# Performance work log

Hardware: AMD Instinct MI355X
Metric: run time of the kernel (lower is better)

Reference implementation:

```python
import jax, jax.numpy as jnp
import numpy as np

N, D, R, C_IN = 384, 256, 64, 2
REL_H, NEI_H = 128, 256


def setup_inputs() -> dict:
    key = jax.random.key(0)
    ks = jax.random.split(key, 16)
    inp = {
        "corr_index": jax.random.normal(ks[0], (N, N, C_IN), jnp.float32),
        "nei_index": jax.random.randint(ks[1], (N, N), 0, 2, jnp.int32),
        "nei_num": jax.random.randint(ks[2], (N,), 0, N, jnp.int32),
        "outgate": jax.random.uniform(ks[3], (N, D), jnp.float32),
        "self_h": jax.random.normal(ks[4], (N, D), jnp.float32),
        "self_c": jax.random.normal(ks[5], (N, D), jnp.float32),
        # relativeLayer: 2-layer MLP, relu after both layers (iflastac=True)
        "rel_w1": jax.random.normal(ks[6], (C_IN, REL_H), jnp.float32) * 0.1,
        "rel_b1": jnp.zeros((REL_H,), jnp.float32),
        "rel_w2": jax.random.normal(ks[7], (REL_H, R), jnp.float32) * 0.1,
        "rel_b2": jnp.zeros((R,), jnp.float32),
        # ngate: single Linear(R+2D -> D) + sigmoid
        "ngate_w": jax.random.normal(ks[8], (R + 2 * D, D), jnp.float32) * 0.005,
        "ngate_b": jnp.zeros((D,), jnp.float32),
        # WAr: single Linear(R+2D -> 1), no activation (WAr_ac='')
        "war_w": jax.random.normal(ks[9], (R + 2 * D, 1), jnp.float32) * 0.05,
        "war_b": jnp.zeros((1,), jnp.float32),
        # W_nei: Linear(D->NEI_H)+relu, Linear(NEI_H->D), no last activation
        "wnei_w1": jax.random.normal(ks[10], (D, NEI_H), jnp.float32) * 0.05,
        "wnei_b1": jnp.zeros((NEI_H,), jnp.float32),
        "wnei_w2": jax.random.normal(ks[11], (NEI_H, D), jnp.float32) * 0.05,
        "wnei_b2": jnp.zeros((D,), jnp.float32),
    }
    return inp


def reference(corr_index, nei_index, nei_num, outgate, self_h, self_c,
              rel_w1, rel_b1, rel_w2, rel_b2, ngate_w, ngate_b,
              war_w, war_b, wnei_w1, wnei_b1, wnei_w2, wnei_b2):
    n, d = self_h.shape
    mask = nei_index > 0  # [N, N], pair (i, j)
    # relativeLayer on pairwise relative coords: relu(relu(x W1 + b1) W2 + b2)
    r = jax.nn.relu(jax.nn.relu(corr_index @ rel_w1 + rel_b1) @ rel_w2 + rel_b2)  # [N,N,R]
    # In torch code flat index k = i*N + j: hi_t[k] = self_h[i], nei_inputs[k] = self_h[j]
    h_i = jnp.broadcast_to(self_h[:, None, :], (n, n, d))
    h_j = jnp.broadcast_to(self_h[None, :, :], (n, n, d))
    feat = jnp.concatenate([r, h_i, h_j], axis=-1)  # [N,N,R+2D]
    gate = jax.nn.sigmoid(feat @ ngate_w + ngate_b)  # [N,N,D]
    msg = h_j * gate
    tt = (feat @ war_w + war_b)[..., 0]  # [N,N] attention logits
    # scatter into zero-init matrix, then Pos[Pos==0] = -inf, row softmax
    pos = jnp.where(mask, tt, 0.0)
    pos = jnp.where(pos == 0.0, -jnp.inf, pos)
    pos = jax.nn.softmax(pos, axis=1)  # [N,N]
    # masked, attention-weighted messages; guard NaN from fully-masked rows
    H = jnp.where(mask[:, :, None], msg * pos[:, :, None], 0.0)  # [N,N,D]
    h_sum = jnp.sum(H, axis=1)  # [N,D]
    h_sum = jax.nn.relu(h_sum @ wnei_w1 + wnei_b1) @ wnei_w2 + wnei_b2
    C = h_sum + self_c
    H_out = outgate * jnp.tanh(C)
    return (outgate, H_out, C)
```

## Files before the change

### kernel.cpp

```cpp
#include <hip/hip_runtime.h>
#include <hip/hip_bf16.h>
#include <math.h>

#define N 384
#define D 256
#define R 64
#define RELH 128
#define NN (N*N)
#define ND (N*D)
#define JCHUNK 64
#define NCHUNK (N / JCHUNK)
#define TPB 16
#define LOG2E 1.44269504088896f
#define BHS_STRIDE 132
#define HS_STRIDE 264

typedef _Float16 f16x8 __attribute__((ext_vector_type(8)));
typedef _Float16 f16x2 __attribute__((ext_vector_type(2)));
typedef float f32x4 __attribute__((ext_vector_type(4)));

__device__ __forceinline__ float fast_sigmoid(float x) {
    float e = __builtin_amdgcn_exp2f(-LOG2E * x);
    return __builtin_amdgcn_rcpf(1.f + e);
}
__device__ __forceinline__ float fast_exp(float x) {
    return __builtin_amdgcn_exp2f(LOG2E * x);
}
__device__ __forceinline__ float fast_tanh(float x) {
    float e = __builtin_amdgcn_exp2f(2.f * LOG2E * x);
    return 1.f - 2.f * __builtin_amdgcn_rcpf(1.f + e);
}

__global__ __launch_bounds__(256) void prep_kernel(
        const float* __restrict__ self_h, const float* __restrict__ ngate_w,
        const float* __restrict__ ngate_b, const float* __restrict__ war_w,
        const float* __restrict__ wnei_w1, const float* __restrict__ wnei_w2,
        float* __restrict__ A, float* __restrict__ Bm,
        unsigned int* __restrict__ bh,
        float* __restrict__ u, float* __restrict__ v,
        _Float16* __restrict__ wf,
        _Float16* __restrict__ wf1, _Float16* __restrict__ wf2) {
    int b = blockIdx.x, tid = threadIdx.x;
    int wv = tid >> 6, l = tid & 63;
    int lg = l >> 4, ln = l & 15;

    if (b < 6) {
        int r0 = b * 64 + wv * 16;
        for (int rr = 0; rr < 16; ++rr) {
            int row = r0 + rr;
            float su = 0.f, sv = 0.f;
            #pragma unroll
            for (int k = 0; k < 4; ++k) {
                int d = k * 64 + l;
                float h = self_h[row * D + d];
                su = fmaf(h, war_w[R + d], su);
                sv = fmaf(h, war_w[R + D + d], sv);
            }
            #pragma unroll
            for (int off = 32; off; off >>= 1) {
                su += __shfl_down(su, off);
                sv += __shfl_down(sv, off);
            }
            if (l == 0) { u[row] = su; v[row] = sv; }
        }
    } else if (b < 54) {
        int W = (b - 6) * 4 + wv;
        int m0 = (W >> 3) * 16;
        int cb = (W & 7) * 64;
        const float* wsrc = ngate_w + (size_t)(cb >= 256 ? 320 : 64) * D + (cb & 255);
        f32x4 acc[4];
        #pragma unroll
        for (int nt = 0; nt < 4; ++nt) acc[nt] = (f32x4){0.f, 0.f, 0.f, 0.f};
        #pragma unroll
        for (int s = 0; s < 8; ++s) {
            const float4* hp = (const float4*)&self_h[(size_t)(m0 + ln) * D + s * 32 + lg * 8];
            float4 h0 = hp[0], h1 = hp[1];
            f16x8 af;
            af[0] = (_Float16)h0.x; af[1] = (_Float16)h0.y;
            af[2] = (_Float16)h0.z; af[3] = (_Float16)h0.w;
            af[4] = (_Float16)h1.x; af[5] = (_Float16)h1.y;
            af[6] = (_Float16)h1.z; af[7] = (_Float16)h1.w;
            #pragma unroll
            for (int nt = 0; nt < 4; ++nt) {
                f16x8 bf;
                #pragma unroll
                for (int ii = 0; ii < 8; ++ii)
                    bf[ii] = (_Float16)wsrc[(size_t)(s * 32 + lg * 8 + ii) * D + nt * 16 + ln];
                acc[nt] = __builtin_amdgcn_mfma_f32_16x16x32_f16(af, bf, acc[nt], 0, 0, 0);
            }
        }
        #pragma unroll
        for (int nt = 0; nt < 4; ++nt)
            #pragma unroll
            for (int reg = 0; reg < 4; ++reg) {
                int row = m0 + lg * 4 + reg;
                int col = cb + nt * 16 + ln;
                if (col < 256) {
                    A[row * D + col] = acc[nt][reg] + ngate_b[col];
                } else {
                    int c2 = col - 256;
                    float bmv = acc[nt][reg];
                    Bm[row * D + c2] = bmv;
                    f16x2 pk;
                    pk[0] = (_Float16)bmv;
                    pk[1] = (_Float16)self_h[row * D + c2];
                    bh[row * D + c2] = __builtin_bit_cast(unsigned int, pk);
                }
            }
    } else if (b < 62) {
        int blkEq = (b - 54) * 4 + wv;
        int s = blkEq >> 4, t = blkEq & 15;
        #pragma unroll
        for (int ii = 0; ii < 8; ++ii) {
            float w = ngate_w[(s * 32 + lg * 8 + ii) * D + t * 16 + ln];
            wf[((size_t)(s * 16 + t) * 64 + l) * 8 + ii] = (_Float16)w;
        }
    } else {
        int base = ((b - 62) * 4 + wv) * 4;
        #pragma unroll
        for (int k = 0; k < 4; ++k) {
            int T = base + k;
            int mat = T >> 7, rem = T & 127;
            int s = rem >> 4, t = rem & 15;
            const float* wsrc = mat ? wnei_w2 : wnei_w1;
            _Float16* dst = mat ? wf2 : wf1;
            #pragma unroll
            for (int ii = 0; ii < 8; ++ii) {
                float w = wsrc[(size_t)(s * 32 + lg * 8 + ii) * D + t * 16 + ln];
                dst[((size_t)(s * 16 + t) * 64 + l) * 8 + ii] = (_Float16)w;
            }
        }
    }
}

__global__ __launch_bounds__(384) void ttsm_kernel(
        const float* __restrict__ corr,
        const float* __restrict__ rel_w1, const float* __restrict__ rel_b1,
        const float* __restrict__ rel_w2, const float* __restrict__ rel_b2,
        const float* __restrict__ war_w, const float* __restrict__ v,
        const int* __restrict__ nei,
        float* __restrict__ pos, _Float16* __restrict__ rc) {
    __shared__ float ttrow[N];
    __shared__ float red[6];
    __shared__ float sM, sS;
    int i = blockIdx.x, tid = threadIdx.x;
    int wv = tid >> 6, l = tid & 63;
    int lg = l >> 4, ln = l & 15;

    f16x8 bfr[4][4];
    #pragma unroll
    for (int s = 0; s < 4; ++s)
        #pragma unroll
        for (int nt = 0; nt < 4; ++nt)
            #pragma unroll
            for (int ii = 0; ii < 8; ++ii)
                bfr[s][nt][ii] = (_Float16)rel_w2[(s * 32 + lg * 8 + ii) * R + nt * 16 + ln];
    float w10[4][8], w11[4][8], b1v[4][8];
    #pragma unroll
    for (int s = 0; s < 4; ++s)
        #pragma unroll
        for (int ii = 0; ii < 8; ++ii) {
            int hk = s * 32 + lg * 8 + ii;
            w10[s][ii] = rel_w1[hk];
            w11[s][ii] = rel_w1[RELH + hk];
            b1v[s][ii] = rel_b1[hk];
        }
    float b2r[4], warw[4];
    #pragma unroll
    for (int nt = 0; nt < 4; ++nt) {
        b2r[nt]  = rel_b2[nt * 16 + ln];
        warw[nt] = war_w[nt * 16 + ln];
    }

    #pragma unroll
    for (int t = 0; t < 4; ++t) {
        int j0 = wv * 64 + t * 16;
        int P0 = i * N + j0;
        float2 x = ((const float2*)corr)[P0 + ln];
        f16x8 af[4];
        #pragma unroll
        for (int s = 0; s < 4; ++s)
            #pragma unroll
            for (int ii = 0; ii < 8; ++ii) {
                float h = fmaxf(0.f, fmaf(x.y, w11[s][ii], fmaf(x.x, w10[s][ii], b1v[s][ii])));
                af[s][ii] = (_Float16)h;
            }
        f32x4 c[4];
        #pragma unroll
        for (int nt = 0; nt < 4; ++nt) c[nt] = (f32x4){0.f, 0.f, 0.f, 0.f};
        #pragma unroll
        for (int nt = 0; nt < 4; ++nt)
            #pragma unroll
            for (int s = 0; s < 4; ++s)
                c[nt] = __builtin_amdgcn_mfma_f32_16x16x32_f16(af[s], bfr[s][nt], c[nt], 0, 0, 0);
        float tpart[4] = {0.f, 0.f, 0.f, 0.f};
        #pragma unroll
        for (int nt = 0; nt < 4; ++nt)
            #pragma unroll
            for (int reg = 0; reg < 4; ++reg) {
                float rv = fmaxf(0.f, c[nt][reg] + b2r[nt]);
                int m = lg * 4 + reg;
                rc[(size_t)(P0 + m) * R + nt * 16 + ln] = (_Float16)rv;
                tpart[reg] = fmaf(rv, warw[nt], tpart[reg]);
            }
        #pragma unroll
        for (int reg = 0; reg < 4; ++reg) {
            float tsum = tpart[reg];
            #pragma unroll
            for (int off = 8; off; off >>= 1) tsum += __shfl_xor(tsum, off, 16);
            tpart[reg] = tsum;
        }
        if (ln == 0) {
            #pragma unroll
            for (int reg = 0; reg < 4; ++reg) {
                int j = j0 + lg * 4 + reg;
                ttrow[j] = tpart[reg] + v[j];
            }
        }
    }
    __syncthreads();

    float tv = ttrow[tid];
    bool va = (nei[i * N + tid] > 0) && (tv != 0.f);
    float m = va ? tv : -INFINITY;
    #pragma unroll
    for (int off = 32; off; off >>= 1) m = fmaxf(m, __shfl_down(m, off));
    if (l == 0) red[wv] = m;
    __syncthreads();
    if (tid == 0) {
        float mm = red[0];
        #pragma unroll
        for (int k = 1; k < 6; ++k) mm = fmaxf(mm, red[k]);
        sM = mm;
    }
    __syncthreads();
    float M = sM;
    float e = 0.f;
    if (va && M != -INFINITY) e = fast_exp(tv - M);
    float sum = e;
    #pragma unroll
    for (int off = 32; off; off >>= 1) sum += __shfl_down(sum, off);
    if (l == 0) red[wv] = sum;
    __syncthreads();
    if (tid == 0) {
        float ss = red[0];
        #pragma unroll
        for (int k = 1; k < 6; ++k) ss += red[k];
        sS = ss;
    }
    __syncthreads();
    float rden = (sS > 0.f) ? __builtin_amdgcn_rcpf(sS) : 0.f;
    pos[i * N + tid] = va ? e * rden : 0.f;
}

__global__ __launch_bounds__(256) void tt_valu_kernel(
        const float* __restrict__ corr,
        const float* __restrict__ rel_w1, const float* __restrict__ rel_b1,
        const float* __restrict__ rel_w2, const float* __restrict__ rel_b2,
        const float* __restrict__ war_w, const float* __restrict__ war_b,
        const float* __restrict__ u, const float* __restrict__ v,
        float* __restrict__ tt) {
    __shared__ __align__(16) float h1s[4][RELH];
    int tid = threadIdx.x, w = tid >> 6, l = tid & 63;
    float w1a0 = rel_w1[l],      w1a1 = rel_w1[RELH + l];
    float w1b0 = rel_w1[64 + l], w1b1 = rel_w1[RELH + 64 + l];
    float b1a = rel_b1[l], b1b = rel_b1[64 + l];
    float b2v = rel_b2[l], warw = war_w[l], wb = war_b[0];
    int pbase = blockIdx.x * TPB;
    #pragma unroll
    for (int it = 0; it < TPB / 4; ++it) {
        int p = pbase + it * 4 + w;
        int i = p / N, j = p - i * N;
        float2 x = *(const float2*)(corr + p * 2);
        h1s[w][l]      = fmaxf(0.f, fmaf(x.y, w1a1, fmaf(x.x, w1a0, b1a)));
        h1s[w][l + 64] = fmaxf(0.f, fmaf(x.y, w1b1, fmaf(x.x, w1b0, b1b)));
        float c0 = b2v, c1 = 0.f, c2 = 0.f, c3 = 0.f;
        const float4* hv = (const float4*)h1s[w];
        #pragma unroll
        for (int k4 = 0; k4 < RELH / 4; ++k4) {
            float4 h = hv[k4];
            c0 = fmaf(h.x, rel_w2[(k4 * 4 + 0) * R + l], c0);
            c1 = fmaf(h.y, rel_w2[(k4 * 4 + 1) * R + l], c1);
            c2 = fmaf(h.z, rel_w2[(k4 * 4 + 2) * R + l], c2);
            c3 = fmaf(h.w, rel_w2[(k4 * 4 + 3) * R + l], c3);
        }
        float rm = fmaxf(0.f, (c0 + c1) + (c2 + c3));
        float part = rm * warw;
        for (int off = 32; off; off >>= 1) part += __shfl_down(part, off);
        if (l == 0) tt[p] = part + u[i] + v[j] + wb;
    }
}

__global__ void softmax_kernel(const float* __restrict__ tt,
                               const int* __restrict__ nei,
                               float* __restrict__ pos) {
    __shared__ float red[4];
    __shared__ float sM, sS;
    int i = blockIdx.x, tid = threadIdx.x;
    float tv[2]; bool valid[2];
    float m = -INFINITY;
    for (int s = 0; s < 2; ++s) {
        int j = tid + s * 256;
        valid[s] = false; tv[s] = 0.f;
        if (j < N) {
            float t = tt[i * N + j];
            bool va = (nei[i * N + j] > 0) && (t != 0.f);
            tv[s] = t; valid[s] = va;
            if (va) m = fmaxf(m, t);
        }
    }
    for (int off = 32; off; off >>= 1) m = fmaxf(m, __shfl_down(m, off));
    if ((tid & 63) == 0) red[tid >> 6] = m;
    __syncthreads();
    if (tid == 0) sM = fmaxf(fmaxf(red[0], red[1]), fmaxf(red[2], red[3]));
    __syncthreads();
    float M = sM;
    float e[2] = {0.f, 0.f};
    float sum = 0.f;
    if (M != -INFINITY) {
        for (int s = 0; s < 2; ++s)
            if (valid[s]) { e[s] = fast_exp(tv[s] - M); sum += e[s]; }
    }
    for (int off = 32; off; off >>= 1) sum += __shfl_down(sum, off);
    if ((tid & 63) == 0) red[tid >> 6] = sum;
    __syncthreads();
    if (tid == 0) sS = red[0] + red[1] + red[2] + red[3];
    __syncthreads();
    float rden = (sS > 0.f) ? __builtin_amdgcn_rcpf(sS) : 0.f;
    for (int s = 0; s < 2; ++s) {
        int j = tid + s * 256;
        if (j < N) pos[i * N + j] = valid[s] ? e[s] * rden : 0.f;
    }
}

__global__ __launch_bounds__(256, 2) void gate_mfma_kernel(
        const _Float16* __restrict__ rc16, const _Float16* __restrict__ wf,
        const float* __restrict__ A, const unsigned int* __restrict__ bh,
        const float* __restrict__ pos, float* __restrict__ partial) {
    __shared__ unsigned int bhs[64 * BHS_STRIDE];
    int itile = blockIdx.x, jc = blockIdx.y, dh = blockIdx.z;
    int jbase = jc * JCHUNK;
    int tid = threadIdx.x, wv = tid >> 6, l = tid & 63;
    int lg = l >> 4, ln = l & 15;
    int i = itile * 4 + wv;

    {
        const uint4* src = (const uint4*)bh;
        #pragma unroll
        for (int s = 0; s < 8; ++s) {
            int f4 = tid + s * 256;
            int row = f4 >> 5, c4 = f4 & 31;
            uint4 vv = src[(size_t)(jbase + row) * (D / 4) + dh * 32 + c4];
            *(uint4*)&bhs[row * BHS_STRIDE + c4 * 4] = vv;
        }
    }

    f16x8 bf[2][8];
    #pragma unroll
    for (int s = 0; s < 2; ++s)
        #pragma unroll
        for (int dt = 0; dt < 8; ++dt)
            bf[s][dt] = *(const f16x8*)&wf[((size_t)(s * 16 + dh * 8 + dt) * 64 + l) * 8];

    float based[8];
    #pragma unroll
    for (int dt = 0; dt < 8; ++dt)
        based[dt] = A[i * D + dh * 128 + dt * 16 + ln];

    float pj[4][4];
    #pragma unroll
    for (int jt = 0; jt < 4; ++jt)
        #pragma unroll
        for (int reg = 0; reg < 4; ++reg)
            pj[jt][reg] = pos[i * N + jbase + jt * 16 + lg * 4 + reg];

    __syncthreads();

    float acc[8] = {0.f, 0.f, 0.f, 0.f, 0.f, 0.f, 0.f, 0.f};
    #pragma unroll
    for (int jt = 0; jt < 4; ++jt) {
        f16x8 af[2];
        #pragma unroll
        for (int s = 0; s < 2; ++s)
            af[s] = *(const f16x8*)&rc16[(size_t)(i * N + jbase + jt * 16 + ln) * R + s * 32 + lg * 8];
        f32x4 c[8];
        #pragma unroll
        for (int dt = 0; dt < 8; ++dt) c[dt] = (f32x4){0.f, 0.f, 0.f, 0.f};
        #pragma unroll
        for (int dt = 0; dt < 8; ++dt)
            #pragma unroll
            for (int s = 0; s < 2; ++s)
                c[dt] = __builtin_amdgcn_mfma_f32_16x16x32_f16(af[s], bf[s][dt], c[dt], 0, 0, 0);
        #pragma unroll
        for (int reg = 0; reg < 4; ++reg) {
            int jl = jt * 16 + lg * 4 + reg;
            float p = pj[jt][reg];
            #pragma unroll
            for (int dt = 0; dt < 8; ++dt) {
                unsigned int uu = bhs[jl * BHS_STRIDE + dt * 16 + ln];
                f16x2 bhv = __builtin_bit_cast(f16x2, uu);
                float logit = c[dt][reg] + based[dt] + (float)bhv[0];
                float g = fast_sigmoid(logit);
                acc[dt] = fmaf(p * g, (float)bhv[1], acc[dt]);
            }
        }
    }
    #pragma unroll
    for (int dt = 0; dt < 8; ++dt) {
        float a = acc[dt];
        a += __shfl_xor(a, 16);
        a += __shfl_xor(a, 32);
        acc[dt] = a;
    }
    if (lg == 0) {
        #pragma unroll
        for (int dt = 0; dt < 8; ++dt)
            partial[(size_t)(jc * N + i) * D + dh * 128 + dt * 16 + ln] = acc[dt];
    }
}

__global__ void gate_norc_kernel(const float* __restrict__ corr,
                            const float* __restrict__ rel_w1, const float* __restrict__ rel_b1,
                            const float* __restrict__ rel_w2, const float* __restrict__ rel_b2,
                            const float* __restrict__ ngate_w,
                            const float* __restrict__ A, const float* __restrict__ Bm,
                            const float* __restrict__ pos, const float* __restrict__ self_h,
                            float* __restrict__ partial) {
    __shared__ __align__(16) float h1[4][RELH];
    __shared__ __align__(16) float rs[4][R];
    __shared__ float wsh[4];
    int i = blockIdx.x, tid = threadIdx.x;
    int jbase = blockIdx.y * JCHUNK;
    int w = tid >> 6, l = tid & 63;
    ((float*)rs)[tid] = 0.f;
    float base = A[i * D + tid];
    float acc = 0.f;
    for (int j0 = jbase; j0 < jbase + JCHUNK; j0 += 4) {
        int j = j0 + w;
        int p = i * N + j;
        float wt = pos[p];
        if (l == 0) wsh[w] = wt;
        if (wt != 0.f) {
            float x0 = corr[p * 2], x1 = corr[p * 2 + 1];
            h1[w][l]      = fmaxf(0.f, fmaf(x1, rel_w1[RELH + l],      fmaf(x0, rel_w1[l],      rel_b1[l])));
            h1[w][l + 64] = fmaxf(0.f, fmaf(x1, rel_w1[RELH + l + 64], fmaf(x0, rel_w1[l + 64], rel_b1[l + 64])));
        }
        __syncthreads();
        if (wsh[w] != 0.f) {
            float c0 = rel_b2[l], c1 = 0.f, c2 = 0.f, c3 = 0.f;
            const float4* hv = (const float4*)h1[w];
            #pragma unroll 8
            for (int k4 = 0; k4 < RELH / 4; ++k4) {
                float4 h = hv[k4];
                int k = k4 * 4;
                c0 = fmaf(h.x, rel_w2[k * R + l], c0);
                c1 = fmaf(h.y, rel_w2[(k + 1) * R + l], c1);
                c2 = fmaf(h.z, rel_w2[(k + 2) * R + l], c2);
                c3 = fmaf(h.w, rel_w2[(k + 3) * R + l], c3);
            }
            rs[w][l] = fmaxf(0.f, (c0 + c1) + (c2 + c3));
        }
        __syncthreads();
        #pragma unroll
        for (int ww = 0; ww < 4; ++ww) {
            float wtj = wsh[ww];
            if (wtj != 0.f) {
                int jj = j0 + ww;
                const float4* rv = (const float4*)rs[ww];
                float l0 = 0.f, l1 = 0.f, l2 = 0.f, l3 = 0.f;
                #pragma unroll 4
                for (int m4 = 0; m4 < R / 4; ++m4) {
                    float4 r4 = rv[m4];
                    int m = m4 * 4;
                    l0 = fmaf(r4.x, ngate_w[m * D + tid], l0);
                    l1 = fmaf(r4.y, ngate_w[(m + 1) * D + tid], l1);
                    l2 = fmaf(r4.z, ngate_w[(m + 2) * D + tid], l2);
                    l3 = fmaf(r4.w, ngate_w[(m + 3) * D + tid], l3);
                }
                float logit = base + Bm[jj * D + tid] + ((l0 + l1) + (l2 + l3));
                float g = fast_sigmoid(logit);
                acc = fmaf(wtj * self_h[jj * D + tid], g, acc);
            }
        }
        __syncthreads();
    }
    partial[(blockIdx.y * N + i) * D + tid] = acc;
}

__global__ __launch_bounds__(256, 2) void final_mfma_kernel(
        const float* __restrict__ partial,
        const _Float16* __restrict__ wf1, const _Float16* __restrict__ wf2,
        const float* __restrict__ wnei_b1, const float* __restrict__ wnei_b2,
        const float* __restrict__ self_c, const float* __restrict__ outgate,
        float* __restrict__ out) {
    __shared__ _Float16 hs16[16][HS_STRIDE];
    __shared__ _Float16 hid16[16][HS_STRIDE];
    int i0 = blockIdx.x * 16;
    int tid = threadIdx.x, wv = tid >> 6, l = tid & 63;
    int lg = l >> 4, ln = l & 15;

    #pragma unroll
    for (int s = 0; s < 4; ++s) {
        int f4 = tid + s * 256;
        int row = f4 >> 6, c4 = f4 & 63;
        float4 a = {0.f, 0.f, 0.f, 0.f};
        #pragma unroll
        for (int c = 0; c < NCHUNK; ++c) {
            float4 p = ((const float4*)partial)[(size_t)(c * N + i0 + row) * (D / 4) + c4];
            a.x += p.x; a.y += p.y; a.z += p.z; a.w += p.w;
        }
        hs16[row][c4 * 4 + 0] = (_Float16)a.x;
        hs16[row][c4 * 4 + 1] = (_Float16)a.y;
        hs16[row][c4 * 4 + 2] = (_Float16)a.z;
        hs16[row][c4 * 4 + 3] = (_Float16)a.w;
    }
    __syncthreads();

    {
        f32x4 c1[4];
        #pragma unroll
        for (int dt = 0; dt < 4; ++dt) c1[dt] = (f32x4){0.f, 0.f, 0.f, 0.f};
        #pragma unroll
        for (int s = 0; s < 8; ++s) {
            f16x8 a = *(const f16x8*)&hs16[ln][s * 32 + lg * 8];
            #pragma unroll
            for (int dt = 0; dt < 4; ++dt) {
                f16x8 bfv = *(const f16x8*)&wf1[((size_t)(s * 16 + wv * 4 + dt) * 64 + l) * 8];
                c1[dt] = __builtin_amdgcn_mfma_f32_16x16x32_f16(a, bfv, c1[dt], 0, 0, 0);
            }
        }
        #pragma unroll
        for (int dt = 0; dt < 4; ++dt) {
            int col = wv * 64 + dt * 16 + ln;
            float b1 = wnei_b1[col];
            #pragma unroll
            for (int reg = 0; reg < 4; ++reg)
                hid16[lg * 4 + reg][col] = (_Float16)fmaxf(0.f, c1[dt][reg] + b1);
        }
    }
    __syncthreads();

    {
        f32x4 c2[4];
        #pragma unroll
        for (int dt = 0; dt < 4; ++dt) c2[dt] = (f32x4){0.f, 0.f, 0.f, 0.f};
        #pragma unroll
        for (int s = 0; s < 8; ++s) {
            f16x8 a = *(const f16x8*)&hid16[ln][s * 32 + lg * 8];
            #pragma unroll
            for (int dt = 0; dt < 4; ++dt) {
                f16x8 bfv = *(const f16x8*)&wf2[((size_t)(s * 16 + wv * 4 + dt) * 64 + l) * 8];
                c2[dt] = __builtin_amdgcn_mfma_f32_16x16x32_f16(a, bfv, c2[dt], 0, 0, 0);
            }
        }
        #pragma unroll
        for (int dt = 0; dt < 4; ++dt) {
            int col = wv * 64 + dt * 16 + ln;
            float b2 = wnei_b2[col];
            #pragma unroll
            for (int reg = 0; reg < 4; ++reg) {
                int row = i0 + lg * 4 + reg;
                int idx = row * D + col;
                float C = c2[dt][reg] + b2 + self_c[idx];
                float og = outgate[idx];
                out[idx] = og;
                out[ND + idx] = og * fast_tanh(C);
                out[2 * ND + idx] = C;
            }
        }
    }
}

extern "C" void kernel_launch(void* const* d_in, const int* in_sizes, int n_in,
                              void* d_out, int out_size, void* d_ws, size_t ws_size,
                              hipStream_t stream) {
    const float* corr    = (const float*)d_in[0];
    const int*   nei     = (const int*)d_in[1];
    const float* outg    = (const float*)d_in[3];
    const float* self_h  = (const float*)d_in[4];
    const float* self_c  = (const float*)d_in[5];
    const float* rel_w1  = (const float*)d_in[6];
    const float* rel_b1  = (const float*)d_in[7];
    const float* rel_w2  = (const float*)d_in[8];
    const float* rel_b2  = (const float*)d_in[9];
    const float* ngate_w = (const float*)d_in[10];
    const float* ngate_b = (const float*)d_in[11];
    const float* war_w   = (const float*)d_in[12];
    const float* war_b   = (const float*)d_in[13];
    const float* wnei_w1 = (const float*)d_in[14];
    const float* wnei_b1 = (const float*)d_in[15];
    const float* wnei_w2 = (const float*)d_in[16];
    const float* wnei_b2 = (const float*)d_in[17];

    float* ws      = (float*)d_ws;
    float* tt      = ws;
    float* pos     = ws + NN;
    float* A       = ws + 2 * NN;
    float* Bm      = ws + 2 * NN + ND;
    float* u       = ws + 2 * NN + 2 * ND;
    float* v       = u + N;
    float* partial = v + N;
    unsigned int* bh = (unsigned int*)(partial + NCHUNK * ND);
    float* tail    = (float*)(bh + ND);
    _Float16* rc16 = (_Float16*)tail;
    _Float16* wf   = rc16 + (size_t)NN * R;
    _Float16* wf1  = wf + 2 * 16 * 64 * 8;
    _Float16* wf2  = wf1 + 8 * 16 * 64 * 8;
    size_t base_floats = (size_t)(2 * NN + 3 * ND + 2 * N + NCHUNK * ND);
    size_t f16_count = (size_t)NN * R + (2 + 8 + 8) * 16 * 64 * 8;
    size_t need = (base_floats + f16_count / 2 + 16) * sizeof(float);
    bool use_rc = ws_size >= need;
    float* out = (float*)d_out;

    prep_kernel<<<78, 256, 0, stream>>>(self_h, ngate_w, ngate_b, war_w,
                                        wnei_w1, wnei_w2,
                                        A, Bm, bh, u, v, wf, wf1, wf2);
    if (use_rc) {
        ttsm_kernel<<<N, 384, 0, stream>>>(corr, rel_w1, rel_b1, rel_w2, rel_b2,
                                           war_w, v, nei, pos, rc16);
        dim3 ggrid(N / 4, NCHUNK, 2);
        gate_mfma_kernel<<<ggrid, 256, 0, stream>>>(rc16, wf, A, bh, pos, partial);
    } else {
        tt_valu_kernel<<<NN / TPB, 256, 0, stream>>>(corr, rel_w1, rel_b1, rel_w2, rel_b2,
                                                     war_w, war_b, u, v, tt);
        softmax_kernel<<<N, 256, 0, stream>>>(tt, nei, pos);
        dim3 ggrid(N, NCHUNK);
        gate_norc_kernel<<<ggrid, 256, 0, stream>>>(corr, rel_w1, rel_b1, rel_w2, rel_b2,
                                                    ngate_w, A, Bm, pos, self_h,
                                                    partial);
    }
    final_mfma_kernel<<<N / 16, 256, 0, stream>>>(partial, wf1, wf2, wnei_b1, wnei_b2,
                                                  self_c, outg, out);
}
```

Baseline: 70.97 us.

## Fuse relative MLP, softmax and gate aggregation into one per-row kernel

Merges the ttsm and gate_mfma kernels into a single kernel with one block per row i. The block keeps the relative-feature tile for all j in XOR-swizzled LDS instead of writing an N*N*R f16 buffer to global memory and reading it back. The softmax weights stay in shared memory and the block writes final h_sum directly, so the partial-sum reduction over chunks is no longer needed. In exchange, the grid is only N blocks with about 48KB of LDS each, which lowers parallelism. The bh tile is now read from global/L2 without LDS staging, and the rel_w2 fragments are pre-packed in prep and reloaded from global.

```diff
diff --git a/kernel.cpp b/kernel.cpp
--- a/kernel.cpp
+++ b/kernel.cpp
@@ -12,7 +12,6 @@
 #define NCHUNK (N / JCHUNK)
 #define TPB 16
 #define LOG2E 1.44269504088896f
-#define BHS_STRIDE 132
 #define HS_STRIDE 264
 
 typedef _Float16 f16x8 __attribute__((ext_vector_type(8)));
@@ -35,11 +34,13 @@
         const float* __restrict__ self_h, const float* __restrict__ ngate_w,
         const float* __restrict__ ngate_b, const float* __restrict__ war_w,
         const float* __restrict__ wnei_w1, const float* __restrict__ wnei_w2,
+        const float* __restrict__ rel_w2,
         float* __restrict__ A, float* __restrict__ Bm,
         unsigned int* __restrict__ bh,
         float* __restrict__ u, float* __restrict__ v,
         _Float16* __restrict__ wf,
-        _Float16* __restrict__ wf1, _Float16* __restrict__ wf2) {
+        _Float16* __restrict__ wf1, _Float16* __restrict__ wf2,
+        _Float16* __restrict__ wfr) {
     int b = blockIdx.x, tid = threadIdx.x;
     int wv = tid >> 6, l = tid & 63;
     int lg = l >> 4, ln = l & 15;
@@ -115,7 +116,7 @@
             float w = ngate_w[(s * 32 + lg * 8 + ii) * D + t * 16 + ln];
             wf[((size_t)(s * 16 + t) * 64 + l) * 8 + ii] = (_Float16)w;
         }
-    } else {
+    } else if (b < 78) {
         int base = ((b - 62) * 4 + wv) * 4;
         #pragma unroll
         for (int k = 0; k < 4; ++k) {
@@ -130,31 +131,38 @@
                 dst[((size_t)(s * 16 + t) * 64 + l) * 8 + ii] = (_Float16)w;
             }
         }
-    }
-}
-
-__global__ __launch_bounds__(384) void ttsm_kernel(
+    } else {
+        #pragma unroll
+        for (int k = 0; k < 4; ++k) {
+            int T = wv * 4 + k;
+            int s = T >> 2, nt = T & 3;
+            #pragma unroll
+            for (int ii = 0; ii < 8; ++ii) {
+                float w = rel_w2[(size_t)(s * 32 + lg * 8 + ii) * R + nt * 16 + ln];
+                wfr[((size_t)(s * 4 + nt) * 64 + l) * 8 + ii] = (_Float16)w;
+            }
+        }
+    }
+}
+
+__global__ __launch_bounds__(256) void fused_kernel(
         const float* __restrict__ corr,
         const float* __restrict__ rel_w1, const float* __restrict__ rel_b1,
-        const float* __restrict__ rel_w2, const float* __restrict__ rel_b2,
+        const float* __restrict__ rel_b2,
         const float* __restrict__ war_w, const float* __restrict__ v,
         const int* __restrict__ nei,
-        float* __restrict__ pos, _Float16* __restrict__ rc) {
+        const _Float16* __restrict__ wfr, const _Float16* __restrict__ wf,
+        const float* __restrict__ A, const unsigned int* __restrict__ bh,
+        float* __restrict__ hsum) {
+    __shared__ __align__(16) _Float16 rlds[N * R];
     __shared__ float ttrow[N];
-    __shared__ float red[6];
+    __shared__ float red[4];
     __shared__ float sM, sS;
     int i = blockIdx.x, tid = threadIdx.x;
     int wv = tid >> 6, l = tid & 63;
     int lg = l >> 4, ln = l & 15;
-
-    f16x8 bfr[4][4];
-    #pragma unroll
-    for (int s = 0; s < 4; ++s)
-        #pragma unroll
-        for (int nt = 0; nt < 4; ++nt)
-            #pragma unroll
-            for (int ii = 0; ii < 8; ++ii)
-                bfr[s][nt][ii] = (_Float16)rel_w2[(s * 32 + lg * 8 + ii) * R + nt * 16 + ln];
+    char* rbase = (char*)rlds;
+
     float w10[4][8], w11[4][8], b1v[4][8];
     #pragma unroll
     for (int s = 0; s < 4; ++s)
@@ -173,10 +181,9 @@
     }
 
     #pragma unroll
-    for (int t = 0; t < 4; ++t) {
-        int j0 = wv * 64 + t * 16;
-        int P0 = i * N + j0;
-        float2 x = ((const float2*)corr)[P0 + ln];
+    for (int t = 0; t < 6; ++t) {
+        int j0 = (wv * 6 + t) * 16;
+        float2 x = ((const float2*)corr)[(size_t)i * N + j0 + ln];
         f16x8 af[4];
         #pragma unroll
         for (int s = 0; s < 4; ++s)
@@ -191,16 +198,19 @@
         #pragma unroll
         for (int nt = 0; nt < 4; ++nt)
             #pragma unroll
-            for (int s = 0; s < 4; ++s)
-                c[nt] = __builtin_amdgcn_mfma_f32_16x16x32_f16(af[s], bfr[s][nt], c[nt], 0, 0, 0);
+            for (int s = 0; s < 4; ++s) {
+                f16x8 bfv = *(const f16x8*)&wfr[((size_t)(s * 4 + nt) * 64 + l) * 8];
+                c[nt] = __builtin_amdgcn_mfma_f32_16x16x32_f16(af[s], bfv, c[nt], 0, 0, 0);
+            }
         float tpart[4] = {0.f, 0.f, 0.f, 0.f};
         #pragma unroll
         for (int nt = 0; nt < 4; ++nt)
             #pragma unroll
             for (int reg = 0; reg < 4; ++reg) {
                 float rv = fmaxf(0.f, c[nt][reg] + b2r[nt]);
-                int m = lg * 4 + reg;
-                rc[(size_t)(P0 + m) * R + nt * 16 + ln] = (_Float16)rv;
+                int j = j0 + lg * 4 + reg;
+                int off = (j * 128 + (nt * 16 + ln) * 2) ^ ((j & 7) << 4);
+                *(_Float16*)(rbase + off) = (_Float16)rv;
                 tpart[reg] = fmaf(rv, warw[nt], tpart[reg]);
             }
         #pragma unroll
@@ -220,37 +230,97 @@
     }
     __syncthreads();
 
-    float tv = ttrow[tid];
-    bool va = (nei[i * N + tid] > 0) && (tv != 0.f);
-    float m = va ? tv : -INFINITY;
-    #pragma unroll
-    for (int off = 32; off; off >>= 1) m = fmaxf(m, __shfl_down(m, off));
-    if (l == 0) red[wv] = m;
-    __syncthreads();
-    if (tid == 0) {
-        float mm = red[0];
-        #pragma unroll
-        for (int k = 1; k < 6; ++k) mm = fmaxf(mm, red[k]);
-        sM = mm;
-    }
-    __syncthreads();
-    float M = sM;
-    float e = 0.f;
-    if (va && M != -INFINITY) e = fast_exp(tv - M);
-    float sum = e;
-    #pragma unroll
-    for (int off = 32; off; off >>= 1) sum += __shfl_down(sum, off);
-    if (l == 0) red[wv] = sum;
-    __syncthreads();
-    if (tid == 0) {
-        float ss = red[0];
-        #pragma unroll
-        for (int k = 1; k < 6; ++k) ss += red[k];
-        sS = ss;
-    }
-    __syncthreads();
-    float rden = (sS > 0.f) ? __builtin_amdgcn_rcpf(sS) : 0.f;
-    pos[i * N + tid] = va ? e * rden : 0.f;
+    {
+        float tv1 = ttrow[tid];
+        bool va1 = (nei[(size_t)i * N + tid] > 0) && (tv1 != 0.f);
+        float tv2 = 0.f; bool va2 = false;
+        if (tid < N - 256) {
+            tv2 = ttrow[tid + 256];
+            va2 = (nei[(size_t)i * N + tid + 256] > 0) && (tv2 != 0.f);
+        }
+        float m = va1 ? tv1 : -INFINITY;
+        if (va2) m = fmaxf(m, tv2);
+        #pragma unroll
+        for (int off = 32; off; off >>= 1) m = fmaxf(m, __shfl_down(m, off));
+        if (l == 0) red[wv] = m;
+        __syncthreads();
+        if (tid == 0) sM = fmaxf(fmaxf(red[0], red[1]), fmaxf(red[2], red[3]));
+        __syncthreads();
+        float M = sM;
+        float e1 = 0.f, e2 = 0.f;
+        if (M != -INFINITY) {
+            if (va1) e1 = fast_exp(tv1 - M);
+            if (va2) e2 = fast_exp(tv2 - M);
+        }
+        float sum = e1 + e2;
+        #pragma unroll
+        for (int off = 32; off; off >>= 1) sum += __shfl_down(sum, off);
+        if (l == 0) red[wv] = sum;
+        __syncthreads();
+        if (tid == 0) sS = red[0] + red[1] + red[2] + red[3];
+        __syncthreads();
+        float rden = (sS > 0.f) ? __builtin_amdgcn_rcpf(sS) : 0.f;
+        ttrow[tid] = va1 ? e1 * rden : 0.f;
+        if (tid < N - 256) ttrow[tid + 256] = va2 ? e2 * rden : 0.f;
+    }
+    __syncthreads();
+
+    f16x8 bf[2][4];
+    #pragma unroll
+    for (int s = 0; s < 2; ++s)
+        #pragma unroll
+        for (int dt = 0; dt < 4; ++dt)
+            bf[s][dt] = *(const f16x8*)&wf[((size_t)(s * 16 + wv * 4 + dt) * 64 + l) * 8];
+    float based[4];
+    #pragma unroll
+    for (int dt = 0; dt < 4; ++dt)
+        based[dt] = A[i * D + wv * 64 + dt * 16 + ln];
+
+    float acc[4] = {0.f, 0.f, 0.f, 0.f};
+    for (int jt = 0; jt < 24; ++jt) {
+        int jb = jt * 16;
+        f16x8 afr[2];
+        #pragma unroll
+        for (int s = 0; s < 2; ++s) {
+            int j = jb + ln;
+            int off = (j * 128 + (s * 64 + lg * 16)) ^ ((j & 7) << 4);
+            afr[s] = *(const f16x8*)(rbase + off);
+        }
+        f32x4 c[4];
+        #pragma unroll
+        for (int dt = 0; dt < 4; ++dt) c[dt] = (f32x4){0.f, 0.f, 0.f, 0.f};
+        #pragma unroll
+        for (int dt = 0; dt < 4; ++dt)
+            #pragma unroll
+            for (int s = 0; s < 2; ++s)
+                c[dt] = __builtin_amdgcn_mfma_f32_16x16x32_f16(afr[s], bf[s][dt], c[dt], 0, 0, 0);
+        #pragma unroll
+        for (int reg = 0; reg < 4; ++reg) {
+            int jj = jb + lg * 4 + reg;
+            float p = ttrow[jj];
+            #pragma unroll
+            for (int dt = 0; dt < 4; ++dt) {
+                int d = wv * 64 + dt * 16 + ln;
+                unsigned int uu = bh[(size_t)jj * D + d];
+                f16x2 bhv = __builtin_bit_cast(f16x2, uu);
+                float logit = c[dt][reg] + based[dt] + (float)bhv[0];
+                float g = fast_sigmoid(logit);
+                acc[dt] = fmaf(p * g, (float)bhv[1], acc[dt]);
+            }
+        }
+    }
+    #pragma unroll
+    for (int dt = 0; dt < 4; ++dt) {
+        float a = acc[dt];
+        a += __shfl_xor(a, 16);
+        a += __shfl_xor(a, 32);
+        acc[dt] = a;
+    }
+    if (lg == 0) {
+        #pragma unroll
+        for (int dt = 0; dt < 4; ++dt)
+            hsum[(size_t)i * D + wv * 64 + dt * 16 + ln] = acc[dt];
+    }
 }
 
 __global__ __launch_bounds__(256) void tt_valu_kernel(
@@ -330,92 +400,6 @@
     for (int s = 0; s < 2; ++s) {
         int j = tid + s * 256;
         if (j < N) pos[i * N + j] = valid[s] ? e[s] * rden : 0.f;
-    }
-}
-
-__global__ __launch_bounds__(256, 2) void gate_mfma_kernel(
-        const _Float16* __restrict__ rc16, const _Float16* __restrict__ wf,
-        const float* __restrict__ A, const unsigned int* __restrict__ bh,
-        const float* __restrict__ pos, float* __restrict__ partial) {
-    __shared__ unsigned int bhs[64 * BHS_STRIDE];
-    int itile = blockIdx.x, jc = blockIdx.y, dh = blockIdx.z;
-    int jbase = jc * JCHUNK;
-    int tid = threadIdx.x, wv = tid >> 6, l = tid & 63;
-    int lg = l >> 4, ln = l & 15;
-    int i = itile * 4 + wv;
-
-    {
-        const uint4* src = (const uint4*)bh;
-        #pragma unroll
-        for (int s = 0; s < 8; ++s) {
-            int f4 = tid + s * 256;
-            int row = f4 >> 5, c4 = f4 & 31;
-            uint4 vv = src[(size_t)(jbase + row) * (D / 4) + dh * 32 + c4];
-            *(uint4*)&bhs[row * BHS_STRIDE + c4 * 4] = vv;
-        }
-    }
-
-    f16x8 bf[2][8];
-    #pragma unroll
-    for (int s = 0; s < 2; ++s)
-        #pragma unroll
-        for (int dt = 0; dt < 8; ++dt)
-            bf[s][dt] = *(const f16x8*)&wf[((size_t)(s * 16 + dh * 8 + dt) * 64 + l) * 8];
-
-    float based[8];
-    #pragma unroll
-    for (int dt = 0; dt < 8; ++dt)
-        based[dt] = A[i * D + dh * 128 + dt * 16 + ln];
-
-    float pj[4][4];
-    #pragma unroll
-    for (int jt = 0; jt < 4; ++jt)
-        #pragma unroll
-        for (int reg = 0; reg < 4; ++reg)
-            pj[jt][reg] = pos[i * N + jbase + jt * 16 + lg * 4 + reg];
-
-    __syncthreads();
-
-    float acc[8] = {0.f, 0.f, 0.f, 0.f, 0.f, 0.f, 0.f, 0.f};
-    #pragma unroll
-    for (int jt = 0; jt < 4; ++jt) {
-        f16x8 af[2];
-        #pragma unroll
-        for (int s = 0; s < 2; ++s)
-            af[s] = *(const f16x8*)&rc16[(size_t)(i * N + jbase + jt * 16 + ln) * R + s * 32 + lg * 8];
-        f32x4 c[8];
-        #pragma unroll
-        for (int dt = 0; dt < 8; ++dt) c[dt] = (f32x4){0.f, 0.f, 0.f, 0.f};
-        #pragma unroll
-        for (int dt = 0; dt < 8; ++dt)
-            #pragma unroll
-            for (int s = 0; s < 2; ++s)
-                c[dt] = __builtin_amdgcn_mfma_f32_16x16x32_f16(af[s], bf[s][dt], c[dt], 0, 0, 0);
-        #pragma unroll
-        for (int reg = 0; reg < 4; ++reg) {
-            int jl = jt * 16 + lg * 4 + reg;
-            float p = pj[jt][reg];
-            #pragma unroll
-            for (int dt = 0; dt < 8; ++dt) {
-                unsigned int uu = bhs[jl * BHS_STRIDE + dt * 16 + ln];
-                f16x2 bhv = __builtin_bit_cast(f16x2, uu);
-                float logit = c[dt][reg] + based[dt] + (float)bhv[0];
-                float g = fast_sigmoid(logit);
-                acc[dt] = fmaf(p * g, (float)bhv[1], acc[dt]);
-            }
-        }
-    }
-    #pragma unroll
-    for (int dt = 0; dt < 8; ++dt) {
-        float a = acc[dt];
-        a += __shfl_xor(a, 16);
-        a += __shfl_xor(a, 32);
-        acc[dt] = a;
-    }
-    if (lg == 0) {
-        #pragma unroll
-        for (int dt = 0; dt < 8; ++dt)
-            partial[(size_t)(jc * N + i) * D + dh * 128 + dt * 16 + ln] = acc[dt];
     }
 }
 
@@ -487,6 +471,7 @@
     partial[(blockIdx.y * N + i) * D + tid] = acc;
 }
 
+template<int CHUNKS>
 __global__ __launch_bounds__(256, 2) void final_mfma_kernel(
         const float* __restrict__ partial,
         const _Float16* __restrict__ wf1, const _Float16* __restrict__ wf2,
@@ -505,7 +490,7 @@
         int row = f4 >> 6, c4 = f4 & 63;
         float4 a = {0.f, 0.f, 0.f, 0.f};
         #pragma unroll
-        for (int c = 0; c < NCHUNK; ++c) {
+        for (int c = 0; c < CHUNKS; ++c) {
             float4 p = ((const float4*)partial)[(size_t)(c * N + i0 + row) * (D / 4) + c4];
             a.x += p.x; a.y += p.y; a.z += p.z; a.w += p.w;
         }
@@ -602,24 +587,25 @@
     float* partial = v + N;
     unsigned int* bh = (unsigned int*)(partial + NCHUNK * ND);
     float* tail    = (float*)(bh + ND);
-    _Float16* rc16 = (_Float16*)tail;
-    _Float16* wf   = rc16 + (size_t)NN * R;
+    _Float16* wf   = (_Float16*)tail;
     _Float16* wf1  = wf + 2 * 16 * 64 * 8;
     _Float16* wf2  = wf1 + 8 * 16 * 64 * 8;
+    _Float16* wfr  = wf2 + 8 * 16 * 64 * 8;
     size_t base_floats = (size_t)(2 * NN + 3 * ND + 2 * N + NCHUNK * ND);
-    size_t f16_count = (size_t)NN * R + (2 + 8 + 8) * 16 * 64 * 8;
+    size_t f16_count = (size_t)(2 + 8 + 8) * 16 * 64 * 8 + 16 * 64 * 8;
     size_t need = (base_floats + f16_count / 2 + 16) * sizeof(float);
-    bool use_rc = ws_size >= need;
+    bool use_fused = ws_size >= need;
     float* out = (float*)d_out;
 
-    prep_kernel<<<78, 256, 0, stream>>>(self_h, ngate_w, ngate_b, war_w,
-                                        wnei_w1, wnei_w2,
-                                        A, Bm, bh, u, v, wf, wf1, wf2);
-    if (use_rc) {
-        ttsm_kernel<<<N, 384, 0, stream>>>(corr, rel_w1, rel_b1, rel_w2, rel_b2,
-                                           war_w, v, nei, pos, rc16);
-        dim3 ggrid(N / 4, NCHUNK, 2);
-        gate_mfma_kernel<<<ggrid, 256, 0, stream>>>(rc16, wf, A, bh, pos, partial);
+    prep_kernel<<<79, 256, 0, stream>>>(self_h, ngate_w, ngate_b, war_w,
+                                        wnei_w1, wnei_w2, rel_w2,
+                                        A, Bm, bh, u, v, wf, wf1, wf2, wfr);
+    if (use_fused) {
+        fused_kernel<<<N, 256, 0, stream>>>(corr, rel_w1, rel_b1, rel_b2,
+                                            war_w, v, nei, wfr, wf, A, bh, partial);
+        final_mfma_kernel<1><<<N / 16, 256, 0, stream>>>(partial, wf1, wf2,
+                                                         wnei_b1, wnei_b2,
+                                                         self_c, outg, out);
     } else {
         tt_valu_kernel<<<NN / TPB, 256, 0, stream>>>(corr, rel_w1, rel_b1, rel_w2, rel_b2,
                                                      war_w, war_b, u, v, tt);
@@ -628,7 +614,8 @@
         gate_norc_kernel<<<ggrid, 256, 0, stream>>>(corr, rel_w1, rel_b1, rel_w2, rel_b2,
                                                     ngate_w, A, Bm, pos, self_h,
                                                     partial);
-    }
-    final_mfma_kernel<<<N / 16, 256, 0, stream>>>(partial, wf1, wf2, wnei_b1, wnei_b2,
-                                                  self_c, outg, out);
-}
+        final_mfma_kernel<NCHUNK><<<N / 16, 256, 0, stream>>>(partial, wf1, wf2,
+                                                              wnei_b1, wnei_b2,
+                                                              self_c, outg, out);
+    }
+}
```

Result: faster. 58.37 us, median of 3 (-17.8%).
